# Kernel optimization log

Hardware: AMD Instinct MI355X
Metric: run time of the kernel (lower is better)

## Reference

```python
import math
import jax, jax.numpy as jnp
import numpy as np

B, S, D, H, DH, R, V = 8, 1024, 1024, 8, 512, 36, 32002  # DH = d_model//2, HD = h*DH = 4096
HD = H * DH
LN_EPS = 1e-5


def setup_inputs() -> dict:
    key = jax.random.key(0)
    ks = jax.random.split(key, 16)

    def n(k, shp, std=0.02):
        return jax.random.normal(k, shp, jnp.float32) * std

    pre_words = jax.random.randint(ks[0], (B, S), 0, V)
    img_features = jax.random.normal(ks[1], (B, R, D), jnp.float32)
    exp_embed = n(ks[2], (V, D)).at[0].set(0.0)  # padding_idx=0
    # id2visual table: sparse nonneg rows over 36 regions; zero rows -> textual tokens
    id2vis = (jax.random.uniform(ks[3], (V, R)) < 0.05).astype(jnp.float32)
    # stacked params for 2 transformer layers; weights stored (in, out) so y = x @ W + b
    wq = n(ks[4], (2, D, HD)); bq = jnp.zeros((2, HD), jnp.float32)
    wk = n(ks[5], (2, D, HD)); bk = jnp.zeros((2, HD), jnp.float32)
    wv = n(ks[6], (2, D, HD)); bv = jnp.zeros((2, HD), jnp.float32)
    wo = n(ks[7], (2, HD, D)); bo = jnp.zeros((2, D), jnp.float32)
    w1 = n(ks[8], (2, D, D)); b1 = jnp.zeros((2, D), jnp.float32)
    w2 = n(ks[9], (2, D, D)); b2 = jnp.zeros((2, D), jnp.float32)
    ln1_g = jnp.ones((2, D), jnp.float32); ln1_b = jnp.zeros((2, D), jnp.float32)
    ln2_g = jnp.ones((2, D), jnp.float32); ln2_b = jnp.zeros((2, D), jnp.float32)
    return dict(pre_words=pre_words, img_features=img_features, exp_embed=exp_embed,
                id2vis=id2vis, wq=wq, bq=bq, wk=wk, bk=bk, wv=wv, bv=bv, wo=wo, bo=bo,
                w1=w1, b1=b1, w2=w2, b2=b2, ln1_g=ln1_g, ln1_b=ln1_b, ln2_g=ln2_g, ln2_b=ln2_b)


def _layer_norm(x, g, b):
    m = x.mean(-1, keepdims=True)
    v = ((x - m) ** 2).mean(-1, keepdims=True)
    return (x - m) / jnp.sqrt(v + LN_EPS) * g + b


def _softmax_one(x):
    # shifted-denominator softmax: exp(x - max) / (1 + sum exp(x - max))
    x = x - x.max(-1, keepdims=True)
    e = jnp.exp(x)
    return e / (1.0 + e.sum(-1, keepdims=True))


def reference(pre_words, img_features, exp_embed, id2vis, wq, bq, wk, bk, wv, bv,
              wo, bo, w1, b1, w2, b2, ln1_g, ln1_b, ln2_g, ln2_b):
    # token embedding: textual (masked to 0 where a visual row exists) + visual bmm
    te = exp_embed[pre_words]                       # (B,S,D)
    vids = id2vis[pre_words]                        # (B,S,R)
    word_mask = vids.sum(-1, keepdims=True) != 0    # (B,S,1)
    ve = jnp.einsum('bsr,brd->bsd', vids, img_features)
    x = jnp.where(word_mask, 0.0, te) + ve          # (B,S,D)

    scale = 1.0 / math.sqrt(DH)
    for i in range(2):  # two structurally identical transformer layers
        h = _layer_norm(x, ln1_g[i], ln1_b[i])
        q = (h @ wq[i] + bq[i]).reshape(B, S, H, DH).transpose(0, 2, 1, 3)
        k = (h @ wk[i] + bk[i]).reshape(B, S, H, DH).transpose(0, 2, 1, 3)
        v = (h @ wv[i] + bv[i]).reshape(B, S, H, DH).transpose(0, 2, 1, 3)
        attn = _softmax_one(jnp.einsum('bhqd,bhkd->bhqk', q, k) * scale)  # (B,H,S,S)
        o = jnp.einsum('bhqk,bhkd->bhqd', attn, v)
        o = o.transpose(0, 2, 1, 3).reshape(B, S, HD)
        x = x + (o @ wo[i] + bo[i])
        f = _layer_norm(x, ln2_g[i], ln2_b[i])
        f = jax.nn.gelu(f @ w1[i] + b1[i], approximate=False) @ w2[i] + b2[i]
        x = x + f
    return x
```

## Files before the change

kernel.cpp:

```cpp
#include <hip/hip_runtime.h>


using u16 = unsigned short;
typedef __attribute__((ext_vector_type(8))) short bf16x8;
typedef __attribute__((ext_vector_type(4))) float f32x4;

__device__ __forceinline__ float b2f(u16 u) {
  union { unsigned int i; float f; } v; v.i = ((unsigned int)u) << 16; return v.f;
}
__device__ __forceinline__ u16 f2b(float f) {
  union { float f; unsigned int i; } v; v.f = f;
  unsigned int i = v.i;
  return (u16)((i + 0x7FFFu + ((i >> 16) & 1u)) >> 16);
}
__device__ __forceinline__ float gelu_f(float x) {
  return 0.5f * x * (1.f + erff(x * 0.70710678118654752f));
}
__device__ __forceinline__ void async16(void* lds, const void* g) {
  __builtin_amdgcn_global_load_lds((const __attribute__((address_space(1))) void*)g,
                                   (__attribute__((address_space(3))) void*)lds, 16, 0, 0);
}
__device__ __forceinline__ void storeC(float* p, float v) { *p = v; }
__device__ __forceinline__ void storeC(u16* p, float v) { *p = f2b(v); }

__global__ __launch_bounds__(256) void embed_k(
    const int* __restrict__ words, const float* __restrict__ img,
    const float* __restrict__ emb, const float* __restrict__ id2v,
    float* __restrict__ x)
{
  __shared__ float vs[36];
  int tok = blockIdx.x, b = tok >> 10, t = threadIdx.x;
  int wd = words[tok];
  if (t < 36) vs[t] = id2v[(size_t)wd * 36 + t];
  __syncthreads();
  bool any = false;
#pragma unroll
  for (int r = 0; r < 36; ++r) any = any || (vs[r] != 0.f);
#pragma unroll
  for (int i = 0; i < 4; ++i) {
    int d = t + (i << 8);
    float acc = 0.f;
    for (int r = 0; r < 36; ++r) {
      float vv = vs[r];
      if (vv != 0.f) acc += vv * img[((size_t)(b * 36 + r) << 10) + d];
    }
    float te = any ? 0.f : emb[((size_t)wd << 10) + d];
    x[((size_t)tok << 10) + d] = te + acc;
  }
}

__global__ __launch_bounds__(256) void ln_k(
    const float* __restrict__ x, u16* __restrict__ out,
    const float* __restrict__ g, const float* __restrict__ bb)
{
  __shared__ float red[4];
  int row = blockIdx.x, t = threadIdx.x;
  const float4 xv = *(const float4*)(x + ((size_t)row << 10) + (t << 2));
  float s = xv.x + xv.y + xv.z + xv.w;
#pragma unroll
  for (int o = 32; o; o >>= 1) s += __shfl_xor(s, o, 64);
  if ((t & 63) == 0) red[t >> 6] = s;
  __syncthreads();
  s = red[0] + red[1] + red[2] + red[3];
  float mean = s * 0.0009765625f;
  float dx = xv.x - mean, dy = xv.y - mean, dz = xv.z - mean, dw = xv.w - mean;
  float q = dx * dx + dy * dy + dz * dz + dw * dw;
  __syncthreads();
#pragma unroll
  for (int o = 32; o; o >>= 1) q += __shfl_xor(q, o, 64);
  if ((t & 63) == 0) red[t >> 6] = q;
  __syncthreads();
  q = red[0] + red[1] + red[2] + red[3];
  float rstd = rsqrtf(q * 0.0009765625f + 1e-5f);
  const float4 gv = *(const float4*)(g + (t << 2));
  const float4 bv = *(const float4*)(bb + (t << 2));
  ushort4 o4;
  o4.x = f2b(dx * rstd * gv.x + bv.x);
  o4.y = f2b(dy * rstd * gv.y + bv.y);
  o4.z = f2b(dz * rstd * gv.z + bv.z);
  o4.w = f2b(dw * rstd * gv.w + bv.w);
  *(ushort4*)(out + ((size_t)row << 10) + (t << 2)) = o4;
}

__global__ __launch_bounds__(256) void sm_k(const u16* __restrict__ S, u16* __restrict__ P)
{
  size_t row = ((size_t)blockIdx.x << 2) + (threadIdx.x >> 6);
  const int lane = threadIdx.x & 63;
  const u16* sr = S + (row << 10) + (lane << 4);
  ushort4 sv[4];
#pragma unroll
  for (int i = 0; i < 4; ++i) sv[i] = *(const ushort4*)(sr + (i << 2));
  float v[16];
#pragma unroll
  for (int i = 0; i < 4; ++i) {
    v[4 * i + 0] = b2f(sv[i].x); v[4 * i + 1] = b2f(sv[i].y);
    v[4 * i + 2] = b2f(sv[i].z); v[4 * i + 3] = b2f(sv[i].w);
  }
  float m = v[0];
#pragma unroll
  for (int i = 1; i < 16; ++i) m = fmaxf(m, v[i]);
#pragma unroll
  for (int o = 32; o; o >>= 1) m = fmaxf(m, __shfl_xor(m, o, 64));
  float s = 0.f;
#pragma unroll
  for (int i = 0; i < 16; ++i) { v[i] = __expf(v[i] - m); s += v[i]; }
#pragma unroll
  for (int o = 32; o; o >>= 1) s += __shfl_xor(s, o, 64);
  const float inv = 1.f / (1.f + s);
  u16* pr = P + (row << 10) + (lane << 4);
#pragma unroll
  for (int i = 0; i < 4; ++i) {
    ushort4 pv;
    pv.x = f2b(v[4 * i + 0] * inv); pv.y = f2b(v[4 * i + 1] * inv);
    pv.z = f2b(v[4 * i + 2] * inv); pv.w = f2b(v[4 * i + 3] * inv);
    *(ushort4*)(pr + (i << 2)) = pv;
  }
}

__global__ __launch_bounds__(256) void tr_k(
    const float* __restrict__ src, u16* __restrict__ dst, int ls, int ld)
{
  __shared__ u16 tile[64][65];
  int c0 = blockIdx.x << 6, r0 = blockIdx.y << 6;
  int tx = threadIdx.x & 63, ty0 = threadIdx.x >> 6;
#pragma unroll
  for (int i = 0; i < 16; ++i) {
    int ty = (ty0 << 4) + i;
    tile[ty][tx] = f2b(src[(size_t)(r0 + ty) * ls + (c0 + tx)]);
  }
  __syncthreads();
#pragma unroll
  for (int i = 0; i < 16; ++i) {
    int ty = (ty0 << 4) + i;
    dst[(size_t)(c0 + ty) * ld + (r0 + tx)] = tile[tx][ty];
  }
}

template <typename CT, int ACT, int BIAS, int RESID, int SPLIT>
__global__ __launch_bounds__(512, 1) void gemm8p(
    const u16* __restrict__ A, const u16* __restrict__ Bt,
    CT* __restrict__ C, const float* __restrict__ bias,
    const float* __restrict__ resid,
    int M, int N, int K, int lda, int ldb, int ldc, float scale,
    int zbase, int zdiv, int ga, int gb, int gc,
    long long aS1, long long aS2, long long bS1, long long bS2,
    long long cS1, long long cS2,
    const float* __restrict__ bias2, CT* __restrict__ C2)
{
  __shared__ u16 lA[2][256 * 64];
  __shared__ u16 lB[2][256 * 64];
  const int nwg = gridDim.x * gridDim.y;
  const int id = blockIdx.y * gridDim.x + blockIdx.x;
  const int qq = nwg >> 3, rr8 = nwg & 7;
  const int xcd = id & 7, off = id >> 3;
  const int swz = (xcd < rr8 ? xcd * (qq + 1) : rr8 * (qq + 1) + (xcd - rr8) * qq) + off;
  const int bx = swz % gridDim.x, by = swz / gridDim.x;

  long long lz = blockIdx.z;
  long long gz = zbase + lz;
  long long zA = ga ? gz : lz, zB = gb ? gz : lz, zC = gc ? gz : lz;
  size_t aOff = (size_t)((zA / zdiv) * aS1 + (zA % zdiv) * aS2);
  size_t bOff = (size_t)((zB / zdiv) * bS1 + (zB % zdiv) * bS2);
  size_t cOff = (size_t)((zC / zdiv) * cS1 + (zC % zdiv) * cS2);
  const int m0 = by << 8, n0 = bx << 8;
  const int tid = threadIdx.x, lane = tid & 63, w = tid >> 6;
  const int wm = w >> 2, wn = w & 3;
  const int srow8 = lane >> 3;
  const int schunk = (lane & 7) ^ srow8;
  const int fr = lane & 15, hi = lane >> 4;
  const int so0 = ((hi ^ (fr & 7)) << 3);
  const int so1 = (((4 + hi) ^ (fr & 7)) << 3);
  const int aRow = ((wm << 7) + fr) << 6;
  const int bRow = ((wn << 6) + fr) << 6;

  f32x4 acc[8][4];
#pragma unroll
  for (int mi = 0; mi < 8; ++mi)
#pragma unroll
    for (int ni = 0; ni < 4; ++ni) acc[mi][ni] = 0.f;

  const u16* Ab = A + aOff;
  const u16* Bb = Bt + bOff;

  auto ST_B = [&](int buf, int k0) {
#pragma unroll
    for (int s = 0; s < 4; ++s) {
      const int rb = (s << 6) + (w << 3);
      async16(&lB[buf][rb << 6], Bb + (size_t)(n0 + rb + srow8) * ldb + (k0 + (schunk << 3)));
    }
  };
  auto ST_A02 = [&](int buf, int k0) {
#pragma unroll
    for (int s = 0; s < 4; s += 2) {
      const int rb = (s << 6) + (w << 3);
      async16(&lA[buf][rb << 6], Ab + (size_t)(m0 + rb + srow8) * lda + (k0 + (schunk << 3)));
    }
  };
  auto ST_A13 = [&](int buf, int k0) {
#pragma unroll
    for (int s = 1; s < 4; s += 2) {
      const int rb = (s << 6) + (w << 3);
      async16(&lA[buf][rb << 6], Ab + (size_t)(m0 + rb + srow8) * lda + (k0 + (schunk << 3)));
    }
  };

  const int nt = K >> 6;
  ST_B(0, 0); ST_A02(0, 0); ST_A13(0, 0);
  ST_B(1, 64); ST_A02(1, 64);

  for (int t = 0; t < nt; ++t) {
    const int cur = t & 1;
    if (t + 1 < nt) asm volatile("s_waitcnt vmcnt(6)" ::: "memory");
    else            asm volatile("s_waitcnt vmcnt(0)" ::: "memory");
    __builtin_amdgcn_s_barrier();

    const u16* bA0 = &lA[cur][aRow + so0];
    const u16* bA1 = &lA[cur][aRow + so1];
    const u16* bB0 = &lB[cur][bRow + so0];
    const u16* bB1 = &lB[cur][bRow + so1];

    bf16x8 b8[4][2];
    const int kt2 = (t + 2) << 6;
#pragma unroll
    for (int p = 0; p < 4; ++p) {
      if (p == 0) {
#pragma unroll
        for (int ni = 0; ni < 4; ++ni) {
          b8[ni][0] = *(const bf16x8*)(bB0 + ni * 1024);
          b8[ni][1] = *(const bf16x8*)(bB1 + ni * 1024);
        }
      }
      bf16x8 a8[2][2];
#pragma unroll
      for (int i = 0; i < 2; ++i) {
        const int mi = (p << 1) + i;
        a8[i][0] = *(const bf16x8*)(bA0 + mi * 1024);
        a8[i][1] = *(const bf16x8*)(bA1 + mi * 1024);
      }
      if (p == 0) { if (t + 1 < nt) ST_A13(cur ^ 1, (t + 1) << 6); }
      else if (p == 1) { if (t + 2 < nt) ST_B(cur, kt2); }
      else if (p == 2) { if (t + 2 < nt) ST_A02(cur, kt2); }
      __builtin_amdgcn_s_barrier();
      asm volatile("s_waitcnt lgkmcnt(0)" ::: "memory");
      __builtin_amdgcn_sched_barrier(0);
      __builtin_amdgcn_s_setprio(1);
#pragma unroll
      for (int i = 0; i < 2; ++i)
#pragma unroll
        for (int ni = 0; ni < 4; ++ni)
#pragma unroll
          for (int ks = 0; ks < 2; ++ks)
            acc[(p << 1) + i][ni] =
                __builtin_amdgcn_mfma_f32_16x16x32_bf16(a8[i][ks], b8[ni][ks],
                                                        acc[(p << 1) + i][ni], 0, 0, 0);
      __builtin_amdgcn_s_setprio(0);
      __builtin_amdgcn_s_barrier();
    }
  }

  const int r4 = hi << 2, cc = fr;
  const int half = N >> 1;
#pragma unroll
  for (int mi = 0; mi < 8; ++mi) {
#pragma unroll
    for (int ni = 0; ni < 4; ++ni) {
      const int col = n0 + (wn << 6) + (ni << 4) + cc;
      CT* Cd = C;
      int colx = col;
      const float* bp = bias;
      if (SPLIT && col >= half) { Cd = C2; colx = col - half; bp = bias2; }
      float bcol = 0.f;
      if (BIAS == 1) bcol = bp[colx];
#pragma unroll
      for (int j = 0; j < 4; ++j) {
        const int row = m0 + (wm << 7) + (mi << 4) + r4 + j;
        float v = acc[mi][ni][j] * scale + bcol;
        if (BIAS == 2) v += bias[row];
        if (ACT == 1) v = gelu_f(v);
        const size_t idx = cOff + (size_t)row * ldc + colx;
        if (RESID) v += resid[idx];
        storeC(&Cd[idx], v);
      }
    }
  }
}

template <typename CT, int ACT, int BIAS, int RESID>
__global__ __launch_bounds__(512, 1) void gemm8pn(
    const u16* __restrict__ A, const u16* __restrict__ Bt,
    CT* __restrict__ C, const float* __restrict__ bias,
    const float* __restrict__ resid,
    int M, int N, int K, int lda, int ldb, int ldc, float scale)
{
  __shared__ u16 lA[2][128 * 64];
  __shared__ u16 lB[2][256 * 64];
  const int nwg = gridDim.x * gridDim.y;
  const int id = blockIdx.y * gridDim.x + blockIdx.x;
  const int qq = nwg >> 3, rr8 = nwg & 7;
  const int xcd = id & 7, off = id >> 3;
  const int swz = (xcd < rr8 ? xcd * (qq + 1) : rr8 * (qq + 1) + (xcd - rr8) * qq) + off;
  const int bx = swz % gridDim.x, by = swz / gridDim.x;

  const int m0 = by << 7, n0 = bx << 8;
  const int tid = threadIdx.x, lane = tid & 63, w = tid >> 6;
  const int wm = w >> 2, wn = w & 3;
  const int srow8 = lane >> 3;
  const int schunk = (lane & 7) ^ srow8;
  const int fr = lane & 15, hi = lane >> 4;
  const int so0 = ((hi ^ (fr & 7)) << 3);
  const int so1 = (((4 + hi) ^ (fr & 7)) << 3);
  const int aRow = ((wm << 6) + fr) << 6;
  const int bRow = ((wn << 6) + fr) << 6;

  f32x4 acc[4][4];
#pragma unroll
  for (int mi = 0; mi < 4; ++mi)
#pragma unroll
    for (int ni = 0; ni < 4; ++ni) acc[mi][ni] = 0.f;

  auto ST = [&](int buf, int k0) {
#pragma unroll
    for (int s = 0; s < 2; ++s) {
      const int rb = (s << 6) + (w << 3);
      async16(&lA[buf][rb << 6], A + (size_t)(m0 + rb + srow8) * lda + (k0 + (schunk << 3)));
    }
#pragma unroll
    for (int s = 0; s < 4; ++s) {
      const int rb = (s << 6) + (w << 3);
      async16(&lB[buf][rb << 6], Bt + (size_t)(n0 + rb + srow8) * ldb + (k0 + (schunk << 3)));
    }
  };

  const int nt = K >> 6;
  ST(0, 0);
  ST(1, 64);
  for (int t = 0; t < nt; ++t) {
    const int cur = t & 1;
    if (t + 1 < nt) asm volatile("s_waitcnt vmcnt(6)" ::: "memory");
    else            asm volatile("s_waitcnt vmcnt(0)" ::: "memory");
    __builtin_amdgcn_s_barrier();

    const u16* bA0 = &lA[cur][aRow + so0];
    const u16* bA1 = &lA[cur][aRow + so1];
    const u16* bB0 = &lB[cur][bRow + so0];
    const u16* bB1 = &lB[cur][bRow + so1];

    bf16x8 a8[4][2], b8[4][2];
#pragma unroll
    for (int mi = 0; mi < 4; ++mi) {
      a8[mi][0] = *(const bf16x8*)(bA0 + mi * 1024);
      a8[mi][1] = *(const bf16x8*)(bA1 + mi * 1024);
    }
#pragma unroll
    for (int ni = 0; ni < 4; ++ni) {
      b8[ni][0] = *(const bf16x8*)(bB0 + ni * 1024);
      b8[ni][1] = *(const bf16x8*)(bB1 + ni * 1024);
    }
    asm volatile("s_waitcnt lgkmcnt(0)" ::: "memory");
    __builtin_amdgcn_sched_barrier(0);
    __builtin_amdgcn_s_setprio(1);
#pragma unroll
    for (int mi = 0; mi < 4; ++mi)
#pragma unroll
      for (int ni = 0; ni < 4; ++ni)
#pragma unroll
        for (int ks = 0; ks < 2; ++ks)
          acc[mi][ni] = __builtin_amdgcn_mfma_f32_16x16x32_bf16(a8[mi][ks], b8[ni][ks],
                                                               acc[mi][ni], 0, 0, 0);
    __builtin_amdgcn_s_setprio(0);
    if (t + 2 < nt) {
      __builtin_amdgcn_s_barrier();
      ST(cur, (t + 2) << 6);
    }
  }

  const int r4 = hi << 2, cc = fr;
#pragma unroll
  for (int mi = 0; mi < 4; ++mi) {
#pragma unroll
    for (int ni = 0; ni < 4; ++ni) {
      const int col = n0 + (wn << 6) + (ni << 4) + cc;
      float bcol = 0.f;
      if (BIAS == 1) bcol = bias[col];
#pragma unroll
      for (int j = 0; j < 4; ++j) {
        const int row = m0 + (wm << 6) + (mi << 4) + r4 + j;
        float v = acc[mi][ni][j] * scale + bcol;
        if (ACT == 1) v = gelu_f(v);
        const size_t idx = (size_t)row * ldc + col;
        if (RESID) v += resid[idx];
        storeC(&C[idx], v);
      }
    }
  }
}

extern "C" void kernel_launch(void* const* d_in, const int* in_sizes, int n_in,
                              void* d_out, int out_size, void* d_ws, size_t ws_size,
                              hipStream_t stream)
{
  (void)in_sizes; (void)n_in; (void)out_size;
  const int*   pre_words = (const int*)d_in[0];
  const float* img  = (const float*)d_in[1];
  const float* emb  = (const float*)d_in[2];
  const float* id2v = (const float*)d_in[3];
  const float* wq = (const float*)d_in[4];  const float* bq = (const float*)d_in[5];
  const float* wk = (const float*)d_in[6];  const float* bk = (const float*)d_in[7];
  const float* wv = (const float*)d_in[8];  const float* bv = (const float*)d_in[9];
  const float* wo = (const float*)d_in[10]; const float* bo = (const float*)d_in[11];
  const float* w1 = (const float*)d_in[12]; const float* b1 = (const float*)d_in[13];
  const float* w2 = (const float*)d_in[14]; const float* b2 = (const float*)d_in[15];
  const float* ln1g = (const float*)d_in[16]; const float* ln1b = (const float*)d_in[17];
  const float* ln2g = (const float*)d_in[18]; const float* ln2b = (const float*)d_in[19];

  const size_t FIXED = 88080384 + (size_t)(1 << 16);
  int g = 1;
  for (int c = 8; c >= 1; c >>= 1)
    if (FIXED + (size_t)c * 25165824 + 2097152 <= ws_size) { g = c; break; }
  int nc = 1;
  int ncmax = 8 * g > 64 ? 64 : 8 * g;
  for (int c = ncmax; c >= 1; c >>= 1)
    if (FIXED + (size_t)g * 25165824 + (size_t)c * 2097152 <= ws_size) { nc = c; break; }

  char* p = (char*)d_ws;
  auto alloc = [&](size_t bytes) -> void* {
    void* r = (void*)p; p += (bytes + 255) & ~(size_t)255; return r;
  };
  float* x  = (float*)alloc((size_t)8192 * 1024 * 4);
  u16* h    = (u16*)alloc((size_t)8192 * 1024 * 2);
  u16* Qg   = (u16*)alloc((size_t)g * 1024 * 4096 * 2);
  u16* Og   = Qg;
  u16* ff   = Qg;
  u16* Kg   = (u16*)alloc((size_t)g * 1024 * 4096 * 2);
  u16* Vtg  = (u16*)alloc((size_t)g * 4096 * 1024 * 2);
  u16* wqkt = (u16*)alloc((size_t)8192 * 1024 * 2);
  u16* wvt  = (u16*)alloc((size_t)4096 * 1024 * 2);
  u16* wot  = (u16*)alloc((size_t)1024 * 4096 * 2);
  u16* w1t  = (u16*)alloc((size_t)1024 * 1024 * 2);
  u16* w2t  = (u16*)alloc((size_t)1024 * 1024 * 2);
  u16* Sc   = (u16*)alloc((size_t)nc << 21);

  embed_k<<<8192, 256, 0, stream>>>(pre_words, img, emb, id2v, x);

  const float qk_scale = 0.044194173824159216f;
  for (int L = 0; L < 2; ++L) {
    const float* WQ = wq + (size_t)L * 1024 * 4096;
    const float* WK = wk + (size_t)L * 1024 * 4096;
    const float* WV = wv + (size_t)L * 1024 * 4096;
    const float* WO = wo + (size_t)L * 4096 * 1024;
    const float* W1 = w1 + (size_t)L * 1024 * 1024;
    const float* W2 = w2 + (size_t)L * 1024 * 1024;

    tr_k<<<dim3(64, 16), 256, 0, stream>>>(WQ, wqkt, 4096, 1024);
    tr_k<<<dim3(64, 16), 256, 0, stream>>>(WK, wqkt + (size_t)4096 * 1024, 4096, 1024);
    tr_k<<<dim3(64, 16), 256, 0, stream>>>(WV, wvt, 4096, 1024);
    tr_k<<<dim3(16, 64), 256, 0, stream>>>(WO, wot, 1024, 4096);
    tr_k<<<dim3(16, 16), 256, 0, stream>>>(W1, w1t, 1024, 1024);
    tr_k<<<dim3(16, 16), 256, 0, stream>>>(W2, w2t, 1024, 1024);

    ln_k<<<8192, 256, 0, stream>>>(x, h, ln1g + L * 1024, ln1b + L * 1024);

    for (int g0 = 0; g0 < 8; g0 += g) {
      const u16* hg = h + (size_t)g0 * 1048576;
      const int Mg = 1024 * g;
      gemm8p<u16, 0, 1, 0, 1><<<dim3(32, Mg >> 8), 512, 0, stream>>>(
          hg, wqkt, Qg, bq + (size_t)L * 4096, nullptr,
          Mg, 8192, 1024, 1024, 1024, 4096, 1.f,
          0, 1, 0, 0, 0, 0, 0, 0, 0, 0, 0,
          bk + (size_t)L * 4096, Kg);
      gemm8p<u16, 0, 2, 0, 0><<<dim3(4, 16, g), 512, 0, stream>>>(
          wvt, h, Vtg, bv + (size_t)L * 4096, nullptr,
          4096, 1024, 1024, 1024, 1024, 1024, 1.f,
          g0, 1, 0, 1, 0, 0, 0, 1048576LL, 0, 4194304LL, 0,
          nullptr, nullptr);
      for (int c0 = 0; c0 < 8 * g; c0 += nc) {
        gemm8p<u16, 0, 0, 0, 0><<<dim3(4, 4, nc), 512, 0, stream>>>(
            Qg, Kg, Sc, nullptr, nullptr,
            1024, 1024, 512, 4096, 4096, 1024, qk_scale,
            c0, 8, 1, 1, 0,
            4194304LL, 512LL, 4194304LL, 512LL, 8388608LL, 1048576LL,
            nullptr, nullptr);
        sm_k<<<nc << 8, 256, 0, stream>>>(Sc, Sc);
        gemm8p<u16, 0, 0, 0, 0><<<dim3(2, 4, nc), 512, 0, stream>>>(
            Sc, Vtg, Og, nullptr, nullptr,
            1024, 512, 1024, 1024, 1024, 4096, 1.f,
            c0, 8, 0, 1, 1,
            8388608LL, 1048576LL, 4194304LL, 524288LL, 4194304LL, 512LL,
            nullptr, nullptr);
      }
      gemm8pn<float, 0, 1, 1><<<dim3(4, Mg >> 7), 512, 0, stream>>>(
          Og, wot, x + (size_t)g0 * 1048576, bo + (size_t)L * 1024,
          x + (size_t)g0 * 1048576,
          Mg, 1024, 4096, 4096, 4096, 1024, 1.f);
    }

    ln_k<<<8192, 256, 0, stream>>>(x, h, ln2g + L * 1024, ln2b + L * 1024);

    gemm8pn<u16, 1, 1, 0><<<dim3(4, 64), 512, 0, stream>>>(
        h, w1t, ff, b1 + (size_t)L * 1024, nullptr,
        8192, 1024, 1024, 1024, 1024, 1024, 1.f);
    float* cdst = (L == 1) ? (float*)d_out : x;
    gemm8pn<float, 0, 1, 1><<<dim3(4, 64), 512, 0, stream>>>(
        ff, w2t, cdst, b2 + (size_t)L * 1024, x,
        8192, 1024, 1024, 1024, 1024, 1024, 1.f);
  }
}
```

Baseline: 1.504 ms.

## Halve K-tile in 256x256 GEMM and simplify prefetch pipeline; relax LDS waits

Result: slower. 1.620 ms (+7.7%).

```diff
diff --git a/kernel.cpp b/kernel.cpp
--- a/kernel.cpp
+++ b/kernel.cpp
@@ -147,8 +147,8 @@
     long long cS1, long long cS2,
     const float* __restrict__ bias2, CT* __restrict__ C2)
 {
-  __shared__ u16 lA[2][256 * 64];
-  __shared__ u16 lB[2][256 * 64];
+  __shared__ u16 lA[2][256 * 32];
+  __shared__ u16 lB[2][256 * 32];
   const int nwg = gridDim.x * gridDim.y;
   const int id = blockIdx.y * gridDim.x + blockIdx.x;
   const int qq = nwg >> 3, rr8 = nwg & 7;
@@ -165,13 +165,12 @@
   const int m0 = by << 8, n0 = bx << 8;
   const int tid = threadIdx.x, lane = tid & 63, w = tid >> 6;
   const int wm = w >> 2, wn = w & 3;
-  const int srow8 = lane >> 3;
-  const int schunk = (lane & 7) ^ srow8;
+  const int srow = lane >> 2;
+  const int schunk = (lane & 3) ^ (srow & 3);
   const int fr = lane & 15, hi = lane >> 4;
-  const int so0 = ((hi ^ (fr & 7)) << 3);
-  const int so1 = (((4 + hi) ^ (fr & 7)) << 3);
-  const int aRow = ((wm << 7) + fr) << 6;
-  const int bRow = ((wn << 6) + fr) << 6;
+  const int so = ((hi ^ (fr & 3)) << 3);
+  const int aRow = ((wm << 7) + fr) << 5;
+  const int bRow = ((wn << 6) + fr) << 5;
 
   f32x4 acc[8][4];
 #pragma unroll
@@ -182,80 +181,43 @@
   const u16* Ab = A + aOff;
   const u16* Bb = Bt + bOff;
 
-  auto ST_B = [&](int buf, int k0) {
-#pragma unroll
-    for (int s = 0; s < 4; ++s) {
-      const int rb = (s << 6) + (w << 3);
-      async16(&lB[buf][rb << 6], Bb + (size_t)(n0 + rb + srow8) * ldb + (k0 + (schunk << 3)));
+  auto ST = [&](int buf, int k0) {
+#pragma unroll
+    for (int i = 0; i < 2; ++i) {
+      const int rb = (w << 5) + (i << 4);
+      async16(&lA[buf][rb << 5], Ab + (size_t)(m0 + rb + srow) * lda + (k0 + (schunk << 3)));
+      async16(&lB[buf][rb << 5], Bb + (size_t)(n0 + rb + srow) * ldb + (k0 + (schunk << 3)));
     }
   };
-  auto ST_A02 = [&](int buf, int k0) {
-#pragma unroll
-    for (int s = 0; s < 4; s += 2) {
-      const int rb = (s << 6) + (w << 3);
-      async16(&lA[buf][rb << 6], Ab + (size_t)(m0 + rb + srow8) * lda + (k0 + (schunk << 3)));
-    }
-  };
-  auto ST_A13 = [&](int buf, int k0) {
-#pragma unroll
-    for (int s = 1; s < 4; s += 2) {
-      const int rb = (s << 6) + (w << 3);
-      async16(&lA[buf][rb << 6], Ab + (size_t)(m0 + rb + srow8) * lda + (k0 + (schunk << 3)));
-    }
-  };
-
-  const int nt = K >> 6;
-  ST_B(0, 0); ST_A02(0, 0); ST_A13(0, 0);
-  ST_B(1, 64); ST_A02(1, 64);
-
+
+  const int nt = K >> 5;
+  ST(0, 0);
+  ST(1, 32);
   for (int t = 0; t < nt; ++t) {
     const int cur = t & 1;
-    if (t + 1 < nt) asm volatile("s_waitcnt vmcnt(6)" ::: "memory");
+    if (t + 1 < nt) asm volatile("s_waitcnt vmcnt(4)" ::: "memory");
     else            asm volatile("s_waitcnt vmcnt(0)" ::: "memory");
     __builtin_amdgcn_s_barrier();
 
-    const u16* bA0 = &lA[cur][aRow + so0];
-    const u16* bA1 = &lA[cur][aRow + so1];
-    const u16* bB0 = &lB[cur][bRow + so0];
-    const u16* bB1 = &lB[cur][bRow + so1];
-
-    bf16x8 b8[4][2];
-    const int kt2 = (t + 2) << 6;
-#pragma unroll
-    for (int p = 0; p < 4; ++p) {
-      if (p == 0) {
-#pragma unroll
-        for (int ni = 0; ni < 4; ++ni) {
-          b8[ni][0] = *(const bf16x8*)(bB0 + ni * 1024);
-          b8[ni][1] = *(const bf16x8*)(bB1 + ni * 1024);
-        }
-      }
-      bf16x8 a8[2][2];
-#pragma unroll
-      for (int i = 0; i < 2; ++i) {
-        const int mi = (p << 1) + i;
-        a8[i][0] = *(const bf16x8*)(bA0 + mi * 1024);
-        a8[i][1] = *(const bf16x8*)(bA1 + mi * 1024);
-      }
-      if (p == 0) { if (t + 1 < nt) ST_A13(cur ^ 1, (t + 1) << 6); }
-      else if (p == 1) { if (t + 2 < nt) ST_B(cur, kt2); }
-      else if (p == 2) { if (t + 2 < nt) ST_A02(cur, kt2); }
-      __builtin_amdgcn_s_barrier();
-      asm volatile("s_waitcnt lgkmcnt(0)" ::: "memory");
-      __builtin_amdgcn_sched_barrier(0);
-      __builtin_amdgcn_s_setprio(1);
-#pragma unroll
-      for (int i = 0; i < 2; ++i)
-#pragma unroll
-        for (int ni = 0; ni < 4; ++ni)
-#pragma unroll
-          for (int ks = 0; ks < 2; ++ks)
-            acc[(p << 1) + i][ni] =
-                __builtin_amdgcn_mfma_f32_16x16x32_bf16(a8[i][ks], b8[ni][ks],
-                                                        acc[(p << 1) + i][ni], 0, 0, 0);
-      __builtin_amdgcn_s_setprio(0);
-      __builtin_amdgcn_s_barrier();
-    }
+    bf16x8 a8[8], b8[4];
+#pragma unroll
+    for (int mi = 0; mi < 8; ++mi)
+      a8[mi] = *(const bf16x8*)&lA[cur][aRow + mi * 512 + so];
+#pragma unroll
+    for (int ni = 0; ni < 4; ++ni)
+      b8[ni] = *(const bf16x8*)&lB[cur][bRow + ni * 512 + so];
+
+    __builtin_amdgcn_s_setprio(1);
+#pragma unroll
+    for (int mi = 0; mi < 8; ++mi)
+#pragma unroll
+      for (int ni = 0; ni < 4; ++ni)
+        acc[mi][ni] = __builtin_amdgcn_mfma_f32_16x16x32_bf16(a8[mi], b8[ni], acc[mi][ni], 0, 0, 0);
+    __builtin_amdgcn_s_setprio(0);
+
+    asm volatile("s_waitcnt lgkmcnt(0)" ::: "memory");
+    __builtin_amdgcn_s_barrier();
+    if (t + 2 < nt) ST(cur, (t + 2) << 5);
   }
 
   const int r4 = hi << 2, cc = fr;
@@ -356,8 +318,6 @@
       b8[ni][0] = *(const bf16x8*)(bB0 + ni * 1024);
       b8[ni][1] = *(const bf16x8*)(bB1 + ni * 1024);
     }
-    asm volatile("s_waitcnt lgkmcnt(0)" ::: "memory");
-    __builtin_amdgcn_sched_barrier(0);
     __builtin_amdgcn_s_setprio(1);
 #pragma unroll
     for (int mi = 0; mi < 4; ++mi)
@@ -368,6 +328,7 @@
           acc[mi][ni] = __builtin_amdgcn_mfma_f32_16x16x32_bf16(a8[mi][ks], b8[ni][ks],
                                                                acc[mi][ni], 0, 0, 0);
     __builtin_amdgcn_s_setprio(0);
+    asm volatile("s_waitcnt lgkmcnt(0)" ::: "memory");
     if (t + 2 < nt) {
       __builtin_amdgcn_s_barrier();
       ST(cur, (t + 2) << 6);
```

## Fuse V projection into QK GEMM with transposed epilogue store

Applied to the files above, without the earlier changes.

Result: slower. 1.543 ms (+2.6%).

```diff
diff --git a/kernel.cpp b/kernel.cpp
--- a/kernel.cpp
+++ b/kernel.cpp
@@ -145,7 +145,8 @@
     int zbase, int zdiv, int ga, int gb, int gc,
     long long aS1, long long aS2, long long bS1, long long bS2,
     long long cS1, long long cS2,
-    const float* __restrict__ bias2, CT* __restrict__ C2)
+    const float* __restrict__ bias2, CT* __restrict__ C2,
+    const float* __restrict__ bias3, u16* __restrict__ C3)
 {
   __shared__ u16 lA[2][256 * 64];
   __shared__ u16 lB[2][256 * 64];
@@ -168,10 +169,6 @@
   const int srow8 = lane >> 3;
   const int schunk = (lane & 7) ^ srow8;
   const int fr = lane & 15, hi = lane >> 4;
-  const int so0 = ((hi ^ (fr & 7)) << 3);
-  const int so1 = (((4 + hi) ^ (fr & 7)) << 3);
-  const int aRow = ((wm << 7) + fr) << 6;
-  const int bRow = ((wn << 6) + fr) << 6;
 
   f32x4 acc[8][4];
 #pragma unroll
@@ -214,29 +211,30 @@
     else            asm volatile("s_waitcnt vmcnt(0)" ::: "memory");
     __builtin_amdgcn_s_barrier();
 
-    const u16* bA0 = &lA[cur][aRow + so0];
-    const u16* bA1 = &lA[cur][aRow + so1];
-    const u16* bB0 = &lB[cur][bRow + so0];
-    const u16* bB1 = &lB[cur][bRow + so1];
-
     bf16x8 b8[4][2];
     const int kt2 = (t + 2) << 6;
 #pragma unroll
     for (int p = 0; p < 4; ++p) {
       if (p == 0) {
 #pragma unroll
-        for (int ni = 0; ni < 4; ++ni) {
-          b8[ni][0] = *(const bf16x8*)(bB0 + ni * 1024);
-          b8[ni][1] = *(const bf16x8*)(bB1 + ni * 1024);
-        }
+        for (int ni = 0; ni < 4; ++ni)
+#pragma unroll
+          for (int ks = 0; ks < 2; ++ks) {
+            const int R = (wn << 6) + (ni << 4) + fr;
+            const int q = (ks << 2) + hi;
+            b8[ni][ks] = *(const bf16x8*)&lB[cur][(R << 6) + ((q ^ (R & 7)) << 3)];
+          }
       }
       bf16x8 a8[2][2];
 #pragma unroll
-      for (int i = 0; i < 2; ++i) {
-        const int mi = (p << 1) + i;
-        a8[i][0] = *(const bf16x8*)(bA0 + mi * 1024);
-        a8[i][1] = *(const bf16x8*)(bA1 + mi * 1024);
-      }
+      for (int i = 0; i < 2; ++i)
+#pragma unroll
+        for (int ks = 0; ks < 2; ++ks) {
+          const int mi = (p << 1) + i;
+          const int R = (wm << 7) + (mi << 4) + fr;
+          const int q = (ks << 2) + hi;
+          a8[i][ks] = *(const bf16x8*)&lA[cur][(R << 6) + ((q ^ (R & 7)) << 3)];
+        }
       if (p == 0) { if (t + 1 < nt) ST_A13(cur ^ 1, (t + 1) << 6); }
       else if (p == 1) { if (t + 2 < nt) ST_B(cur, kt2); }
       else if (p == 2) { if (t + 2 < nt) ST_A02(cur, kt2); }
@@ -259,27 +257,39 @@
   }
 
   const int r4 = hi << 2, cc = fr;
-  const int half = N >> 1;
 #pragma unroll
   for (int mi = 0; mi < 8; ++mi) {
 #pragma unroll
     for (int ni = 0; ni < 4; ++ni) {
       const int col = n0 + (wn << 6) + (ni << 4) + cc;
-      CT* Cd = C;
-      int colx = col;
-      const float* bp = bias;
-      if (SPLIT && col >= half) { Cd = C2; colx = col - half; bp = bias2; }
-      float bcol = 0.f;
-      if (BIAS == 1) bcol = bp[colx];
-#pragma unroll
-      for (int j = 0; j < 4; ++j) {
-        const int row = m0 + (wm << 7) + (mi << 4) + r4 + j;
-        float v = acc[mi][ni][j] * scale + bcol;
-        if (BIAS == 2) v += bias[row];
-        if (ACT == 1) v = gelu_f(v);
-        const size_t idx = cOff + (size_t)row * ldc + colx;
-        if (RESID) v += resid[idx];
-        storeC(&Cd[idx], v);
+      const int row0 = m0 + (wm << 7) + (mi << 4) + r4;
+      if (SPLIT && col >= 8192) {
+        const int colx = col - 8192;
+        const float b3 = bias3[colx];
+        ushort4 st;
+        st.x = f2b(acc[mi][ni][0] + b3);
+        st.y = f2b(acc[mi][ni][1] + b3);
+        st.z = f2b(acc[mi][ni][2] + b3);
+        st.w = f2b(acc[mi][ni][3] + b3);
+        const size_t vb = ((size_t)(row0 >> 10)) * 4194304 +
+                          (size_t)colx * 1024 + (row0 & 1023);
+        *(ushort4*)(C3 + vb) = st;
+      } else {
+        CT* Cd = C;
+        int colx = col;
+        const float* bp = bias;
+        if (SPLIT && col >= 4096) { Cd = C2; colx = col - 4096; bp = bias2; }
+        float bcol = 0.f;
+        if (BIAS == 1) bcol = bp[colx];
+#pragma unroll
+        for (int j = 0; j < 4; ++j) {
+          const int row = row0 + j;
+          float v = acc[mi][ni][j] * scale + bcol;
+          if (ACT == 1) v = gelu_f(v);
+          const size_t idx = cOff + (size_t)row * ldc + colx;
+          if (RESID) v += resid[idx];
+          storeC(&Cd[idx], v);
+        }
       }
     }
   }
@@ -433,8 +443,7 @@
   u16* ff   = Qg;
   u16* Kg   = (u16*)alloc((size_t)g * 1024 * 4096 * 2);
   u16* Vtg  = (u16*)alloc((size_t)g * 4096 * 1024 * 2);
-  u16* wqkt = (u16*)alloc((size_t)8192 * 1024 * 2);
-  u16* wvt  = (u16*)alloc((size_t)4096 * 1024 * 2);
+  u16* wqkvt = (u16*)alloc((size_t)12288 * 1024 * 2);
   u16* wot  = (u16*)alloc((size_t)1024 * 4096 * 2);
   u16* w1t  = (u16*)alloc((size_t)1024 * 1024 * 2);
   u16* w2t  = (u16*)alloc((size_t)1024 * 1024 * 2);
@@ -451,9 +460,9 @@
     const float* W1 = w1 + (size_t)L * 1024 * 1024;
     const float* W2 = w2 + (size_t)L * 1024 * 1024;
 
-    tr_k<<<dim3(64, 16), 256, 0, stream>>>(WQ, wqkt, 4096, 1024);
-    tr_k<<<dim3(64, 16), 256, 0, stream>>>(WK, wqkt + (size_t)4096 * 1024, 4096, 1024);
-    tr_k<<<dim3(64, 16), 256, 0, stream>>>(WV, wvt, 4096, 1024);
+    tr_k<<<dim3(64, 16), 256, 0, stream>>>(WQ, wqkvt, 4096, 1024);
+    tr_k<<<dim3(64, 16), 256, 0, stream>>>(WK, wqkvt + (size_t)4096 * 1024, 4096, 1024);
+    tr_k<<<dim3(64, 16), 256, 0, stream>>>(WV, wqkvt + (size_t)8192 * 1024, 4096, 1024);
     tr_k<<<dim3(16, 64), 256, 0, stream>>>(WO, wot, 1024, 4096);
     tr_k<<<dim3(16, 16), 256, 0, stream>>>(W1, w1t, 1024, 1024);
     tr_k<<<dim3(16, 16), 256, 0, stream>>>(W2, w2t, 1024, 1024);
@@ -463,30 +472,26 @@
     for (int g0 = 0; g0 < 8; g0 += g) {
       const u16* hg = h + (size_t)g0 * 1048576;
       const int Mg = 1024 * g;
-      gemm8p<u16, 0, 1, 0, 1><<<dim3(32, Mg >> 8), 512, 0, stream>>>(
-          hg, wqkt, Qg, bq + (size_t)L * 4096, nullptr,
-          Mg, 8192, 1024, 1024, 1024, 4096, 1.f,
+      gemm8p<u16, 0, 1, 0, 1><<<dim3(48, Mg >> 8), 512, 0, stream>>>(
+          hg, wqkvt, Qg, bq + (size_t)L * 4096, nullptr,
+          Mg, 12288, 1024, 1024, 1024, 4096, 1.f,
           0, 1, 0, 0, 0, 0, 0, 0, 0, 0, 0,
-          bk + (size_t)L * 4096, Kg);
-      gemm8p<u16, 0, 2, 0, 0><<<dim3(4, 16, g), 512, 0, stream>>>(
-          wvt, h, Vtg, bv + (size_t)L * 4096, nullptr,
-          4096, 1024, 1024, 1024, 1024, 1024, 1.f,
-          g0, 1, 0, 1, 0, 0, 0, 1048576LL, 0, 4194304LL, 0,
-          nullptr, nullptr);
+          bk + (size_t)L * 4096, Kg,
+          bv + (size_t)L * 4096, Vtg);
       for (int c0 = 0; c0 < 8 * g; c0 += nc) {
         gemm8p<u16, 0, 0, 0, 0><<<dim3(4, 4, nc), 512, 0, stream>>>(
             Qg, Kg, Sc, nullptr, nullptr,
             1024, 1024, 512, 4096, 4096, 1024, qk_scale,
             c0, 8, 1, 1, 0,
             4194304LL, 512LL, 4194304LL, 512LL, 8388608LL, 1048576LL,
-            nullptr, nullptr);
+            nullptr, nullptr, nullptr, nullptr);
         sm_k<<<nc << 8, 256, 0, stream>>>(Sc, Sc);
         gemm8p<u16, 0, 0, 0, 0><<<dim3(2, 4, nc), 512, 0, stream>>>(
             Sc, Vtg, Og, nullptr, nullptr,
             1024, 512, 1024, 1024, 1024, 4096, 1.f,
             c0, 8, 0, 1, 1,
             8388608LL, 1048576LL, 4194304LL, 524288LL, 4194304LL, 512LL,
-            nullptr, nullptr);
+            nullptr, nullptr, nullptr, nullptr);
       }
       gemm8pn<float, 0, 1, 1><<<dim3(4, Mg >> 7), 512, 0, stream>>>(
           Og, wot, x + (size_t)g0 * 1048576, bo + (size_t)L * 1024,
```
